# Performance work log

Hardware: AMD Instinct MI355X
Metric: run time of the kernel (lower is better)

## Reference

```python
import jax, jax.numpy as jnp
import numpy as np
import math

B, S, D, H = 2, 2048, 512, 8
DH = D // H  # 64

def setup_inputs() -> dict:
    key = jax.random.key(0)
    ks = jax.random.split(key, 7)
    x = jax.random.normal(ks[0], (B, S, D), jnp.float32)
    shift = jax.random.normal(ks[1], (B, S, S), jnp.float32)
    mask = jax.random.randint(ks[2], (B, S, S), 0, 2).astype(jnp.float32)
    W = jax.random.normal(ks[3], (3 * D, D), jnp.float32) / math.sqrt(D)
    b = jnp.zeros((3 * D,), jnp.float32)
    Wo = jax.random.normal(ks[4], (D, D), jnp.float32) / math.sqrt(D)
    bo = jnp.zeros((D,), jnp.float32)
    return {"x": x, "shift": shift, "mask": mask, "W": W, "b": b, "Wo": Wo, "bo": bo}

def reference(x, shift, mask, W, b, Wo, bo):
    # qkv projection: (B,S,3D). torch chunk(n_heads) then chunk(3) =>
    # per-head layout is [q_h | k_h | v_h] within each 3*DH-sized slice.
    qkv = x @ W.T + b
    qkv = qkv.reshape(B, S, H, 3, DH)
    qkv = jnp.moveaxis(qkv, (2, 3), (0, 1))  # (H, 3, B, S, DH)
    q, k, v = qkv[:, 0], qkv[:, 1], qkv[:, 2]  # each (H, B, S, DH)

    head_scale = jnp.exp2(-jnp.arange(H, dtype=jnp.float32)).reshape(H, 1, 1, 1)  # 2^-h
    logits = jnp.einsum('hbqd,hbkd->hbqk', q, k) / math.sqrt(DH)
    logits = logits - head_scale * shift[None]          # ALiBi-style per-head shift
    m = mask[None]                                       # (1,B,S,S)
    logits = logits * m - 1e8 * (1.0 - m)
    att = jax.nn.softmax(logits, axis=-1)
    o = jnp.einsum('hbqk,hbkd->hbqd', att, v)            # (H,B,S,DH)
    o = jnp.moveaxis(o, 0, 2).reshape(B, S, D)           # concat heads on last dim
    return o @ Wo.T + bo
```

## Files before the change

### kernel.cpp

```cpp
#include <hip/hip_runtime.h>
#include <math.h>

constexpr int Bc = 2, Sc = 2048, Dc = 512, Hc = 8, DHc = 64;
constexpr int NQKV = 3 * Dc;

typedef unsigned short u16;
typedef unsigned int u32;
typedef __attribute__((ext_vector_type(8))) __bf16 bf16x8;
typedef __attribute__((ext_vector_type(16))) float f32x16;

#define MFMA32 __builtin_amdgcn_mfma_f32_32x32x16_bf16

__device__ inline uint2 splitpack2(float a, float b) {
  u32 ua = __float_as_uint(a), ub = __float_as_uint(b);
  u32 hi = (ub & 0xFFFF0000u) | (ua >> 16);
  float ra = a - __uint_as_float(ua & 0xFFFF0000u);
  float rb = b - __uint_as_float(ub & 0xFFFF0000u);
  u32 lo = (__float_as_uint(rb) & 0xFFFF0000u) | (__float_as_uint(ra) >> 16);
  return uint2{hi, lo};
}
__device__ inline void split1(float v, u16& hi, u16& lo) {
  u32 u = __float_as_uint(v);
  hi = (u16)(u >> 16);
  float r = v - __uint_as_float(u & 0xFFFF0000u);
  lo = (u16)(__float_as_uint(r) >> 16);
}

__global__ __launch_bounds__(256, 2) void gemm1_mfma(
    const float* __restrict__ x, const float* __restrict__ W,
    const float* __restrict__ bias, u16* __restrict__ Qhi,
    u16* __restrict__ Qlo, u16* __restrict__ Khi, u16* __restrict__ Klo,
    u16* __restrict__ Vthi, u16* __restrict__ Vtlo) {
  __shared__ __align__(16) u16 pool[18432];
  const int tid = threadIdx.x;
  const int wave = tid >> 6, lane = tid & 63, l31 = lane & 31, lhi = lane >> 5;
  const int wm = wave >> 1, wn = wave & 1;
  const int m0 = blockIdx.y * 128, n0 = blockIdx.x * 64;

  f32x16 acc[2];
#pragma unroll
  for (int r = 0; r < 16; ++r) {
    acc[0][r] = 0.f;
    acc[1][r] = 0.f;
  }

  for (int k0 = 0; k0 < 512; k0 += 32) {
#pragma unroll
    for (int i = 0; i < 2; ++i) {
      const int g = i * 256 + tid;
      const int m = g >> 2, kg = g & 3;
      const float* src = x + (size_t)(m0 + m) * 512 + k0 + kg * 8;
      const float4 v0 = *(const float4*)src;
      const float4 v1 = *(const float4*)(src + 4);
      const uint2 p0 = splitpack2(v0.x, v0.y), p1 = splitpack2(v0.z, v0.w);
      const uint2 p2 = splitpack2(v1.x, v1.y), p3 = splitpack2(v1.z, v1.w);
      const int row = (kg & 1) * 32 + (m & 31);
      *(uint4*)&pool[((((0 * 4 + (m >> 5)) * 2 + (kg >> 1)) * 64 + row)) * 8] =
          uint4{p0.x, p1.x, p2.x, p3.x};
      *(uint4*)&pool[((((1 * 4 + (m >> 5)) * 2 + (kg >> 1)) * 64 + row)) * 8] =
          uint4{p0.y, p1.y, p2.y, p3.y};
    }
    {
      const int n = tid >> 2, kg = tid & 3;
      const float* src = W + (size_t)(n0 + n) * 512 + k0 + kg * 8;
      const float4 v0 = *(const float4*)src;
      const float4 v1 = *(const float4*)(src + 4);
      const uint2 p0 = splitpack2(v0.x, v0.y), p1 = splitpack2(v0.z, v0.w);
      const uint2 p2 = splitpack2(v1.x, v1.y), p3 = splitpack2(v1.z, v1.w);
      const int row = (kg & 1) * 32 + (n & 31);
      *(uint4*)&pool[8192 +
                     ((((0 * 2 + (n >> 5)) * 2 + (kg >> 1)) * 64 + row)) * 8] =
          uint4{p0.x, p1.x, p2.x, p3.x};
      *(uint4*)&pool[8192 +
                     ((((1 * 2 + (n >> 5)) * 2 + (kg >> 1)) * 64 + row)) * 8] =
          uint4{p0.y, p1.y, p2.y, p3.y};
    }
    __syncthreads();
#pragma unroll
    for (int t = 0; t < 2; ++t) {
      const bf16x8 bh =
          *(const bf16x8*)&pool[8192 + (((0 * 2 + wn) * 2 + t) * 64 + lane) * 8];
      const bf16x8 bl =
          *(const bf16x8*)&pool[8192 + (((1 * 2 + wn) * 2 + t) * 64 + lane) * 8];
#pragma unroll
      for (int ti = 0; ti < 2; ++ti) {
        const bf16x8 ah =
            *(const bf16x8*)&pool[(((0 * 4 + wm * 2 + ti) * 2 + t) * 64 + lane) * 8];
        const bf16x8 al =
            *(const bf16x8*)&pool[(((1 * 4 + wm * 2 + ti) * 2 + t) * 64 + lane) * 8];
        acc[ti] = MFMA32(ah, bh, acc[ti], 0, 0, 0);
        acc[ti] = MFMA32(ah, bl, acc[ti], 0, 0, 0);
        acc[ti] = MFMA32(al, bh, acc[ti], 0, 0, 0);
      }
    }
    __syncthreads();
  }

  const int n = n0 + wn * 32 + l31;
  const float bn = bias[n];
  const int h = n0 / 192;
  const int t3 = (n0 % 192) / 64;
  const int dh = wn * 32 + l31;
  const int batch = m0 >> 11;
  const int s0 = m0 & 2047;
  const int hbq = h * 2 + batch;

#pragma unroll
  for (int ti = 0; ti < 2; ++ti)
#pragma unroll
    for (int r = 0; r < 16; ++r) {
      const int tl = wm * 64 + ti * 32 + (r & 3) + 8 * (r >> 2) + 4 * lhi;
      float val = acc[ti][r] + bn;
      if (t3 == 0) val *= 0.125f;
      u16 hi, lo;
      split1(val, hi, lo);
      pool[tl * 72 + dh] = hi;
      pool[9216 + tl * 72 + dh] = lo;
    }
  __syncthreads();

  u16 *d0, *d1;
  if (t3 == 0) {
    d0 = Qhi;
    d1 = Qlo;
  } else if (t3 == 1) {
    d0 = Khi;
    d1 = Klo;
  } else {
    d0 = Vthi;
    d1 = Vtlo;
  }

  if (t3 != 2) {
    const size_t base = ((size_t)hbq * 2048 + s0) * 64;
#pragma unroll
    for (int p = 0; p < 2; ++p) {
      u16* dst = (p ? d1 : d0) + base;
#pragma unroll
      for (int j = 0; j < 4; ++j) {
        const int g = tid * 32 + j * 8;
        const int token = g >> 6, dh8 = g & 63;
        *(uint4*)(dst + g) = *(const uint4*)&pool[p * 9216 + token * 72 + dh8];
      }
    }
  } else {
    const int d = tid >> 2, tp = (tid & 3) * 32;
#pragma unroll
    for (int p = 0; p < 2; ++p) {
      u16* dst = (p ? d1 : d0) + ((size_t)hbq * 64 + d) * 2048 + s0 + tp;
      u32 w[16];
#pragma unroll
      for (int j = 0; j < 16; ++j) {
        const u16 a = pool[p * 9216 + (tp + 2 * j) * 72 + d];
        const u16 b2 = pool[p * 9216 + (tp + 2 * j + 1) * 72 + d];
        w[j] = (u32)a | ((u32)b2 << 16);
      }
#pragma unroll
      for (int j = 0; j < 4; ++j)
        *(uint4*)(dst + j * 8) =
            uint4{w[4 * j], w[4 * j + 1], w[4 * j + 2], w[4 * j + 3]};
    }
  }
}

constexpr int KF0 = 8320;
constexpr int VF0 = 24704;
constexpr int PF0 = 41088;

__global__ __launch_bounds__(512, 1) void attn_mfma(
    const u16* __restrict__ Qhi, const u16* __restrict__ Qlo,
    const u16* __restrict__ Khi, const u16* __restrict__ Klo,
    const u16* __restrict__ Vthi, const u16* __restrict__ Vtlo,
    const float* __restrict__ shift, const float* __restrict__ mask,
    u16* __restrict__ Othi, u16* __restrict__ Otlo) {
  const int hp = blockIdx.z, b = blockIdx.y, qb = blockIdx.x;
  const int tid = threadIdx.x;
  const int wave = tid >> 6;
  const int hsel = wave >> 2, wq = (wave >> 1) & 1, wk = wave & 1;
  const int lane = tid & 63;
  const int l31 = lane & 31, lhi = lane >> 5;

  __shared__ __align__(16) u16 smem[57472];
  float* SMs = (float*)smem;
  u16* Pw = smem + PF0 + wave * 2048;

  const int head = hp * 2 + hsel;
  const size_t hb = (size_t)head * Bc + b;
  const int ql = wq * 32 + l31;
  const int qg = qb * 64 + ql;

  bf16x8 qf[2][4];
  {
    const size_t qbase = (hb * Sc + qg) * DHc;
#pragma unroll
    for (int t = 0; t < 4; ++t) {
      qf[0][t] = *(const bf16x8*)(Qhi + qbase + t * 16 + lhi * 8);
      qf[1][t] = *(const bf16x8*)(Qlo + qbase + t * 16 + lhi * 8);
    }
  }
  const float hs = exp2f(-(float)head);

  const int smq = tid >> 3, smk = (tid & 7) * 8;
  const float* shr = shift + ((size_t)b * Sc + qb * 64 + smq) * Sc + smk;
  const float* mkr = mask + ((size_t)b * Sc + qb * 64 + smq) * Sc + smk;

  const int kr = lane >> 1, kh2 = lane & 1;
  const size_t kfix = (hb * Sc + wk * 32 + kr) * 64 + kh2 * 32;
  const size_t vfix = (hb * 64 + lane) * 2048 + wk * 32;
  const int vmt = lane >> 5, vdl = lane & 31;

  float m_run = -INFINITY, l_run = 0.f;
  f32x16 o0, o1;
#pragma unroll
  for (int i = 0; i < 16; ++i) {
    o0[i] = 0.f;
    o1[i] = 0.f;
  }

  for (int it = 0; it < 32; ++it) {
    const int kt = it * 64;
    {
      const float4 s0 = *(const float4*)(shr + kt);
      const float4 s1 = *(const float4*)(shr + kt + 4);
      const float4 m0 = *(const float4*)(mkr + kt);
      const float4 m1 = *(const float4*)(mkr + kt + 4);
      float* dst = SMs + (size_t)smk * 65 + smq;
      dst[0 * 65] = (m0.x != 0.f) ? s0.x : 1e13f;
      dst[1 * 65] = (m0.y != 0.f) ? s0.y : 1e13f;
      dst[2 * 65] = (m0.z != 0.f) ? s0.z : 1e13f;
      dst[3 * 65] = (m0.w != 0.f) ? s0.w : 1e13f;
      dst[4 * 65] = (m1.x != 0.f) ? s1.x : 1e13f;
      dst[5 * 65] = (m1.y != 0.f) ? s1.y : 1e13f;
      dst[6 * 65] = (m1.z != 0.f) ? s1.z : 1e13f;
      dst[7 * 65] = (m1.w != 0.f) ? s1.w : 1e13f;
    }
    if (wq == 0) {
      const size_t gb = kfix + (size_t)kt * 64;
#pragma unroll
      for (int c = 0; c < 4; ++c) {
        const int dhc = kh2 * 32 + c * 8;
        const int t = dhc >> 4, lh = (dhc >> 3) & 1;
        *(uint4*)&smem[KF0 + ((((hsel * 2 + 0) * 2 + wk) * 4 + t) * 64 +
                              lh * 32 + kr) * 8] =
            *(const uint4*)(Khi + gb + c * 8);
        *(uint4*)&smem[KF0 + ((((hsel * 2 + 1) * 2 + wk) * 4 + t) * 64 +
                              lh * 32 + kr) * 8] =
            *(const uint4*)(Klo + gb + c * 8);
      }
    } else {
      const size_t gb = vfix + kt;
#pragma unroll
      for (int c = 0; c < 4; ++c) {
        const int t = c >> 1, lh = c & 1;
        *(uint4*)&smem[VF0 + (((((hsel * 2 + 0) * 2 + wk) * 2 + vmt) * 2 + t) *
                                  64 + lh * 32 + vdl) * 8] =
            *(const uint4*)(Vthi + gb + c * 8);
        *(uint4*)&smem[VF0 + (((((hsel * 2 + 1) * 2 + wk) * 2 + vmt) * 2 + t) *
                                  64 + lh * 32 + vdl) * 8] =
            *(const uint4*)(Vtlo + gb + c * 8);
      }
    }
    __syncthreads();

    f32x16 s;
#pragma unroll
    for (int i = 0; i < 16; ++i) s[i] = 0.f;
#pragma unroll
    for (int t = 0; t < 4; ++t) {
      const bf16x8 kh = *(const bf16x8*)&smem[KF0 +
          ((((hsel * 2 + 0) * 2 + wk) * 4 + t) * 64 + lane) * 8];
      const bf16x8 kl = *(const bf16x8*)&smem[KF0 +
          ((((hsel * 2 + 1) * 2 + wk) * 4 + t) * 64 + lane) * 8];
      s = MFMA32(kh, qf[0][t], s, 0, 0, 0);
      s = MFMA32(kh, qf[1][t], s, 0, 0, 0);
      s = MFMA32(kl, qf[0][t], s, 0, 0, 0);
    }

    float p[16];
    float kmax = -INFINITY;
#pragma unroll
    for (int c = 0; c < 4; ++c) {
#pragma unroll
      for (int e = 0; e < 4; ++e) {
        const int kl_ = wk * 32 + c * 8 + lhi * 4 + e;
        const float a = hs * SMs[(size_t)kl_ * 65 + ql];
        const float lg = s[4 * c + e] - a;
        p[4 * c + e] = lg;
        kmax = fmaxf(kmax, lg);
      }
    }
    kmax = fmaxf(kmax, __shfl_xor(kmax, 32, 64));
    const float mnew = fmaxf(m_run, kmax);
    const float alpha = __expf(m_run - mnew);
    float rsum = 0.f;
#pragma unroll
    for (int r = 0; r < 16; ++r) {
      p[r] = __expf(p[r] - mnew);
      rsum += p[r];
    }
    rsum += __shfl_xor(rsum, 32, 64);
    l_run = l_run * alpha + rsum;
    m_run = mnew;
#pragma unroll
    for (int i = 0; i < 16; ++i) {
      o0[i] *= alpha;
      o1[i] *= alpha;
    }

#pragma unroll
    for (int c = 0; c < 4; ++c) {
      const uint2 s01 = splitpack2(p[4 * c + 0], p[4 * c + 1]);
      const uint2 s23 = splitpack2(p[4 * c + 2], p[4 * c + 3]);
      const int t = c >> 1, lh = c & 1;
      const int bi = (t * 64 + lh * 32 + l31) * 8 + lhi * 4;
      *(uint2*)&Pw[bi] = uint2{s01.x, s23.x};
      *(uint2*)&Pw[1024 + bi] = uint2{s01.y, s23.y};
    }

#pragma unroll
    for (int t = 0; t < 2; ++t) {
      const bf16x8 ph = *(const bf16x8*)&Pw[(t * 64 + lane) * 8];
      const bf16x8 pl_ = *(const bf16x8*)&Pw[1024 + (t * 64 + lane) * 8];
      bf16x8 vh = *(const bf16x8*)&smem[VF0 +
          (((((hsel * 2 + 0) * 2 + wk) * 2 + 0) * 2 + t) * 64 + lane) * 8];
      bf16x8 vl = *(const bf16x8*)&smem[VF0 +
          (((((hsel * 2 + 1) * 2 + wk) * 2 + 0) * 2 + t) * 64 + lane) * 8];
      o0 = MFMA32(vh, ph, o0, 0, 0, 0);
      o0 = MFMA32(vh, pl_, o0, 0, 0, 0);
      o0 = MFMA32(vl, ph, o0, 0, 0, 0);
      vh = *(const bf16x8*)&smem[VF0 +
          (((((hsel * 2 + 0) * 2 + wk) * 2 + 1) * 2 + t) * 64 + lane) * 8];
      vl = *(const bf16x8*)&smem[VF0 +
          (((((hsel * 2 + 1) * 2 + wk) * 2 + 1) * 2 + t) * 64 + lane) * 8];
      o1 = MFMA32(vh, ph, o1, 0, 0, 0);
      o1 = MFMA32(vh, pl_, o1, 0, 0, 0);
      o1 = MFMA32(vl, ph, o1, 0, 0, 0);
    }
    __syncthreads();
  }

  float* mL = (float*)(smem + KF0);
  float* lL = mL + 128;
  float* Om = lL + 128;
  if (wk == 1) {
    if (lhi == 0) {
      mL[(hsel * 2 + wq) * 32 + l31] = m_run;
      lL[(hsel * 2 + wq) * 32 + l31] = l_run;
    }
#pragma unroll
    for (int mt = 0; mt < 2; ++mt)
#pragma unroll
      for (int r = 0; r < 16; ++r) {
        const int row = mt * 32 + (r & 3) + 8 * (r >> 2) + 4 * lhi;
        Om[((hsel * 2 + wq) * 64 + row) * 33 + l31] = (mt ? o1[r] : o0[r]);
      }
  }
  __syncthreads();
  if (wk == 0) {
    const float m1 = mL[(hsel * 2 + wq) * 32 + l31];
    const float l1v = lL[(hsel * 2 + wq) * 32 + l31];
    const float mst = fmaxf(m_run, m1);
    const float a0 = __expf(m_run - mst), a1 = __expf(m1 - mst);
    const float inv = 1.f / (a0 * l_run + a1 * l1v);
    const int tok = b * 2048 + qg;
#pragma unroll
    for (int mt = 0; mt < 2; ++mt)
#pragma unroll
      for (int r = 0; r < 16; ++r) {
        const int row = mt * 32 + (r & 3) + 8 * (r >> 2) + 4 * lhi;
        const float val = (a0 * (mt ? o1[r] : o0[r]) +
                           a1 * Om[((hsel * 2 + wq) * 64 + row) * 33 + l31]) *
                          inv;
        const int d = head * 64 + row;
        u16 hi, lo;
        split1(val, hi, lo);
        const size_t idx = ((size_t)(d >> 3) * 4096 + tok) * 8 + (d & 7);
        Othi[idx] = hi;
        Otlo[idx] = lo;
      }
  }
}

__global__ __launch_bounds__(256, 2) void gemm2_mfma(
    const u16* __restrict__ Othi, const u16* __restrict__ Otlo,
    const float* __restrict__ Wo, const float* __restrict__ bo,
    float* __restrict__ out) {
  __shared__ __align__(16) u16 Af[2][2][2][64][8];
  __shared__ __align__(16) u16 Bf[2][2][2][64][8];
  const int tid = threadIdx.x;
  const int wave = tid >> 6, lane = tid & 63, l31 = lane & 31, lhi = lane >> 5;
  const int wm = wave >> 1, wn = wave & 1;
  const int m0 = blockIdx.y * 64, n0 = blockIdx.x * 64;

  f32x16 acc;
#pragma unroll
  for (int r = 0; r < 16; ++r) acc[r] = 0.f;

  for (int k0 = 0; k0 < 512; k0 += 32) {
#pragma unroll
    for (int i = 0; i < 2; ++i) {
      const int f = i * 256 + tid;
      const int p = f >> 8, rem = f & 255, c = rem >> 6, tok = rem & 63;
      const u16* src =
          (p ? Otlo : Othi) + ((size_t)(k0 / 8 + c) * 4096 + m0 + tok) * 8;
      *(uint4*)&Af[p][tok >> 5][c >> 1][(c & 1) * 32 + (tok & 31)][0] =
          *(const uint4*)src;
    }
    {
      const int n = tid >> 2, c = tid & 3;
      const float* src = Wo + (size_t)(n0 + n) * 512 + k0 + c * 8;
      const float4 v0 = *(const float4*)src;
      const float4 v1 = *(const float4*)(src + 4);
      const uint2 q0 = splitpack2(v0.x, v0.y), q1 = splitpack2(v0.z, v0.w);
      const uint2 q2 = splitpack2(v1.x, v1.y), q3 = splitpack2(v1.z, v1.w);
      *(uint4*)&Bf[0][n >> 5][c >> 1][(c & 1) * 32 + (n & 31)][0] =
          uint4{q0.x, q1.x, q2.x, q3.x};
      *(uint4*)&Bf[1][n >> 5][c >> 1][(c & 1) * 32 + (n & 31)][0] =
          uint4{q0.y, q1.y, q2.y, q3.y};
    }
    __syncthreads();
#pragma unroll
    for (int t = 0; t < 2; ++t) {
      const bf16x8 ah = *(const bf16x8*)&Af[0][wm][t][lane][0];
      const bf16x8 al = *(const bf16x8*)&Af[1][wm][t][lane][0];
      const bf16x8 bh = *(const bf16x8*)&Bf[0][wn][t][lane][0];
      const bf16x8 bl = *(const bf16x8*)&Bf[1][wn][t][lane][0];
      acc = MFMA32(ah, bh, acc, 0, 0, 0);
      acc = MFMA32(ah, bl, acc, 0, 0, 0);
      acc = MFMA32(al, bh, acc, 0, 0, 0);
    }
    __syncthreads();
  }

  const int n = n0 + wn * 32 + l31;
  const float bn = bo[n];
#pragma unroll
  for (int r = 0; r < 16; ++r) {
    const int m = m0 + wm * 32 + (r & 3) + 8 * (r >> 2) + 4 * lhi;
    out[(size_t)m * 512 + n] = acc[r] + bn;
  }
}

extern "C" void kernel_launch(void* const* d_in, const int* in_sizes, int n_in,
                              void* d_out, int out_size, void* d_ws,
                              size_t ws_size, hipStream_t stream) {
  const float* x = (const float*)d_in[0];
  const float* shift = (const float*)d_in[1];
  const float* mask = (const float*)d_in[2];
  const float* W = (const float*)d_in[3];
  const float* b = (const float*)d_in[4];
  const float* Wo = (const float*)d_in[5];
  const float* bo = (const float*)d_in[6];
  float* out = (float*)d_out;

  const size_t P = (size_t)Hc * Bc * Sc * DHc;
  u16* ws0 = (u16*)d_ws;
  u16* Qhi = ws0;
  u16* Qlo = ws0 + P;
  u16* Khi = ws0 + 2 * P;
  u16* Klo = ws0 + 3 * P;
  u16* Vthi = ws0 + 4 * P;
  u16* Vtlo = ws0 + 5 * P;
  u16* Othi = ws0 + 6 * P;
  u16* Otlo = ws0 + 7 * P;

  gemm1_mfma<<<dim3(NQKV / 64, (Bc * Sc) / 128), 256, 0, stream>>>(
      x, W, b, Qhi, Qlo, Khi, Klo, Vthi, Vtlo);

  attn_mfma<<<dim3(Sc / 64, Bc, Hc / 2), 512, 0, stream>>>(
      Qhi, Qlo, Khi, Klo, Vthi, Vtlo, shift, mask, Othi, Otlo);

  gemm2_mfma<<<dim3(Dc / 64, (Bc * Sc) / 64), 256, 0, stream>>>(Othi, Otlo, Wo,
                                                                bo, out);
}
```

Before: 291.8 us.

## Split attention blocks to one head each and register-prefetch next tile loads

Attention blocks now process a single head with 4 waves instead of two heads with 8 waves, halving shared memory and allowing two blocks per CU. Global loads of shift, mask and K/V for the next key tile are issued into registers before the current tile's compute and committed to shared memory after. This hides load latency and raises occupancy. The cost is that shift/mask tiles are now fetched once per head rather than shared by two heads, doubling that traffic, plus more register pressure.

```diff
diff --git a/kernel.cpp b/kernel.cpp
--- a/kernel.cpp
+++ b/kernel.cpp
@@ -164,27 +164,26 @@
 }
 
 constexpr int KF0 = 8320;
-constexpr int VF0 = 24704;
-constexpr int PF0 = 41088;
-
-__global__ __launch_bounds__(512, 1) void attn_mfma(
+constexpr int VF0 = 16512;
+constexpr int PF0 = 24704;
+
+__global__ __launch_bounds__(256, 2) void attn_mfma(
     const u16* __restrict__ Qhi, const u16* __restrict__ Qlo,
     const u16* __restrict__ Khi, const u16* __restrict__ Klo,
     const u16* __restrict__ Vthi, const u16* __restrict__ Vtlo,
     const float* __restrict__ shift, const float* __restrict__ mask,
     u16* __restrict__ Othi, u16* __restrict__ Otlo) {
-  const int hp = blockIdx.z, b = blockIdx.y, qb = blockIdx.x;
+  const int head = blockIdx.z, b = blockIdx.y, qb = blockIdx.x;
   const int tid = threadIdx.x;
   const int wave = tid >> 6;
-  const int hsel = wave >> 2, wq = (wave >> 1) & 1, wk = wave & 1;
+  const int wq = wave >> 1, wk = wave & 1;
   const int lane = tid & 63;
   const int l31 = lane & 31, lhi = lane >> 5;
 
-  __shared__ __align__(16) u16 smem[57472];
+  __shared__ __align__(16) u16 smem[32896];
   float* SMs = (float*)smem;
   u16* Pw = smem + PF0 + wave * 2048;
 
-  const int head = hp * 2 + hsel;
   const size_t hb = (size_t)head * Bc + b;
   const int ql = wq * 32 + l31;
   const int qg = qb * 64 + ql;
@@ -200,7 +199,7 @@
   }
   const float hs = exp2f(-(float)head);
 
-  const int smq = tid >> 3, smk = (tid & 7) * 8;
+  const int smq = tid >> 2, smk = (tid & 3) * 16;
   const float* shr = shift + ((size_t)b * Sc + qb * 64 + smq) * Sc + smk;
   const float* mkr = mask + ((size_t)b * Sc + qb * 64 + smq) * Sc + smk;
 
@@ -217,50 +216,71 @@
     o1[i] = 0.f;
   }
 
-  for (int it = 0; it < 32; ++it) {
+  float4 pS[4], pM[4];
+  uint4 pKV[8];
+
+  auto issue = [&](int it) {
     const int kt = it * 64;
-    {
-      const float4 s0 = *(const float4*)(shr + kt);
-      const float4 s1 = *(const float4*)(shr + kt + 4);
-      const float4 m0 = *(const float4*)(mkr + kt);
-      const float4 m1 = *(const float4*)(mkr + kt + 4);
-      float* dst = SMs + (size_t)smk * 65 + smq;
-      dst[0 * 65] = (m0.x != 0.f) ? s0.x : 1e13f;
-      dst[1 * 65] = (m0.y != 0.f) ? s0.y : 1e13f;
-      dst[2 * 65] = (m0.z != 0.f) ? s0.z : 1e13f;
-      dst[3 * 65] = (m0.w != 0.f) ? s0.w : 1e13f;
-      dst[4 * 65] = (m1.x != 0.f) ? s1.x : 1e13f;
-      dst[5 * 65] = (m1.y != 0.f) ? s1.y : 1e13f;
-      dst[6 * 65] = (m1.z != 0.f) ? s1.z : 1e13f;
-      dst[7 * 65] = (m1.w != 0.f) ? s1.w : 1e13f;
+#pragma unroll
+    for (int c = 0; c < 4; ++c) {
+      pS[c] = *(const float4*)(shr + kt + c * 4);
+      pM[c] = *(const float4*)(mkr + kt + c * 4);
     }
     if (wq == 0) {
       const size_t gb = kfix + (size_t)kt * 64;
+#pragma unroll
+      for (int c = 0; c < 4; ++c) {
+        pKV[2 * c] = *(const uint4*)(Khi + gb + c * 8);
+        pKV[2 * c + 1] = *(const uint4*)(Klo + gb + c * 8);
+      }
+    } else {
+      const size_t gb = vfix + kt;
+#pragma unroll
+      for (int c = 0; c < 4; ++c) {
+        pKV[2 * c] = *(const uint4*)(Vthi + gb + c * 8);
+        pKV[2 * c + 1] = *(const uint4*)(Vtlo + gb + c * 8);
+      }
+    }
+  };
+
+  auto commit = [&]() {
+#pragma unroll
+    for (int c = 0; c < 4; ++c) {
+      float* dst = SMs + (size_t)(smk + c * 4) * 65 + smq;
+      dst[0 * 65] = (pM[c].x != 0.f) ? pS[c].x : 1e13f;
+      dst[1 * 65] = (pM[c].y != 0.f) ? pS[c].y : 1e13f;
+      dst[2 * 65] = (pM[c].z != 0.f) ? pS[c].z : 1e13f;
+      dst[3 * 65] = (pM[c].w != 0.f) ? pS[c].w : 1e13f;
+    }
+    if (wq == 0) {
 #pragma unroll
       for (int c = 0; c < 4; ++c) {
         const int dhc = kh2 * 32 + c * 8;
         const int t = dhc >> 4, lh = (dhc >> 3) & 1;
-        *(uint4*)&smem[KF0 + ((((hsel * 2 + 0) * 2 + wk) * 4 + t) * 64 +
-                              lh * 32 + kr) * 8] =
-            *(const uint4*)(Khi + gb + c * 8);
-        *(uint4*)&smem[KF0 + ((((hsel * 2 + 1) * 2 + wk) * 4 + t) * 64 +
-                              lh * 32 + kr) * 8] =
-            *(const uint4*)(Klo + gb + c * 8);
+        *(uint4*)&smem[KF0 +
+                       (((0 * 2 + wk) * 4 + t) * 64 + lh * 32 + kr) * 8] =
+            pKV[2 * c];
+        *(uint4*)&smem[KF0 +
+                       (((1 * 2 + wk) * 4 + t) * 64 + lh * 32 + kr) * 8] =
+            pKV[2 * c + 1];
       }
     } else {
-      const size_t gb = vfix + kt;
 #pragma unroll
       for (int c = 0; c < 4; ++c) {
         const int t = c >> 1, lh = c & 1;
-        *(uint4*)&smem[VF0 + (((((hsel * 2 + 0) * 2 + wk) * 2 + vmt) * 2 + t) *
-                                  64 + lh * 32 + vdl) * 8] =
-            *(const uint4*)(Vthi + gb + c * 8);
-        *(uint4*)&smem[VF0 + (((((hsel * 2 + 1) * 2 + wk) * 2 + vmt) * 2 + t) *
-                                  64 + lh * 32 + vdl) * 8] =
-            *(const uint4*)(Vtlo + gb + c * 8);
-      }
-    }
-    __syncthreads();
+        *(uint4*)&smem[VF0 + ((((0 * 2 + wk) * 2 + vmt) * 2 + t) * 64 +
+                              lh * 32 + vdl) * 8] = pKV[2 * c];
+        *(uint4*)&smem[VF0 + ((((1 * 2 + wk) * 2 + vmt) * 2 + t) * 64 +
+                              lh * 32 + vdl) * 8] = pKV[2 * c + 1];
+      }
+    }
+  };
+
+  issue(0);
+  for (int it = 0; it < 32; ++it) {
+    commit();
+    __syncthreads();
+    if (it < 31) issue(it + 1);
 
     f32x16 s;
 #pragma unroll
@@ -268,9 +288,9 @@
 #pragma unroll
     for (int t = 0; t < 4; ++t) {
       const bf16x8 kh = *(const bf16x8*)&smem[KF0 +
-          ((((hsel * 2 + 0) * 2 + wk) * 4 + t) * 64 + lane) * 8];
+          (((0 * 2 + wk) * 4 + t) * 64 + lane) * 8];
       const bf16x8 kl = *(const bf16x8*)&smem[KF0 +
-          ((((hsel * 2 + 1) * 2 + wk) * 4 + t) * 64 + lane) * 8];
+          (((1 * 2 + wk) * 4 + t) * 64 + lane) * 8];
       s = MFMA32(kh, qf[0][t], s, 0, 0, 0);
       s = MFMA32(kh, qf[1][t], s, 0, 0, 0);
       s = MFMA32(kl, qf[0][t], s, 0, 0, 0);
@@ -322,16 +342,16 @@
       const bf16x8 ph = *(const bf16x8*)&Pw[(t * 64 + lane) * 8];
       const bf16x8 pl_ = *(const bf16x8*)&Pw[1024 + (t * 64 + lane) * 8];
       bf16x8 vh = *(const bf16x8*)&smem[VF0 +
-          (((((hsel * 2 + 0) * 2 + wk) * 2 + 0) * 2 + t) * 64 + lane) * 8];
+          ((((0 * 2 + wk) * 2 + 0) * 2 + t) * 64 + lane) * 8];
       bf16x8 vl = *(const bf16x8*)&smem[VF0 +
-          (((((hsel * 2 + 1) * 2 + wk) * 2 + 0) * 2 + t) * 64 + lane) * 8];
+          ((((1 * 2 + wk) * 2 + 0) * 2 + t) * 64 + lane) * 8];
       o0 = MFMA32(vh, ph, o0, 0, 0, 0);
       o0 = MFMA32(vh, pl_, o0, 0, 0, 0);
       o0 = MFMA32(vl, ph, o0, 0, 0, 0);
       vh = *(const bf16x8*)&smem[VF0 +
-          (((((hsel * 2 + 0) * 2 + wk) * 2 + 1) * 2 + t) * 64 + lane) * 8];
+          ((((0 * 2 + wk) * 2 + 1) * 2 + t) * 64 + lane) * 8];
       vl = *(const bf16x8*)&smem[VF0 +
-          (((((hsel * 2 + 1) * 2 + wk) * 2 + 1) * 2 + t) * 64 + lane) * 8];
+          ((((1 * 2 + wk) * 2 + 1) * 2 + t) * 64 + lane) * 8];
       o1 = MFMA32(vh, ph, o1, 0, 0, 0);
       o1 = MFMA32(vh, pl_, o1, 0, 0, 0);
       o1 = MFMA32(vl, ph, o1, 0, 0, 0);
@@ -340,25 +360,25 @@
   }
 
   float* mL = (float*)(smem + KF0);
-  float* lL = mL + 128;
-  float* Om = lL + 128;
+  float* lL = mL + 64;
+  float* Om = lL + 64;
   if (wk == 1) {
     if (lhi == 0) {
-      mL[(hsel * 2 + wq) * 32 + l31] = m_run;
-      lL[(hsel * 2 + wq) * 32 + l31] = l_run;
+      mL[wq * 32 + l31] = m_run;
+      lL[wq * 32 + l31] = l_run;
     }
 #pragma unroll
     for (int mt = 0; mt < 2; ++mt)
 #pragma unroll
       for (int r = 0; r < 16; ++r) {
         const int row = mt * 32 + (r & 3) + 8 * (r >> 2) + 4 * lhi;
-        Om[((hsel * 2 + wq) * 64 + row) * 33 + l31] = (mt ? o1[r] : o0[r]);
+        Om[(wq * 64 + row) * 33 + l31] = (mt ? o1[r] : o0[r]);
       }
   }
   __syncthreads();
   if (wk == 0) {
-    const float m1 = mL[(hsel * 2 + wq) * 32 + l31];
-    const float l1v = lL[(hsel * 2 + wq) * 32 + l31];
+    const float m1 = mL[wq * 32 + l31];
+    const float l1v = lL[wq * 32 + l31];
     const float mst = fmaxf(m_run, m1);
     const float a0 = __expf(m_run - mst), a1 = __expf(m1 - mst);
     const float inv = 1.f / (a0 * l_run + a1 * l1v);
@@ -369,7 +389,7 @@
       for (int r = 0; r < 16; ++r) {
         const int row = mt * 32 + (r & 3) + 8 * (r >> 2) + 4 * lhi;
         const float val = (a0 * (mt ? o1[r] : o0[r]) +
-                           a1 * Om[((hsel * 2 + wq) * 64 + row) * 33 + l31]) *
+                           a1 * Om[(wq * 64 + row) * 33 + l31]) *
                           inv;
         const int d = head * 64 + row;
         u16 hi, lo;
@@ -467,7 +487,7 @@
   gemm1_mfma<<<dim3(NQKV / 64, (Bc * Sc) / 128), 256, 0, stream>>>(
       x, W, b, Qhi, Qlo, Khi, Klo, Vthi, Vtlo);
 
-  attn_mfma<<<dim3(Sc / 64, Bc, Hc / 2), 512, 0, stream>>>(
+  attn_mfma<<<dim3(Sc / 64, Bc, Hc), 256, 0, stream>>>(
       Qhi, Qlo, Khi, Klo, Vthi, Vtlo, shift, mask, Othi, Otlo);
 
   gemm2_mfma<<<dim3(Dc / 64, (Bc * Sc) / 64), 256, 0, stream>>>(Othi, Otlo, Wo,
```

After: 389.5 us. +33.5%, slower.
